# Kernel optimization log

Hardware: AMD Instinct MI355X
Metric: run time of the kernel (lower is better)

## Reference

```python
import jax, jax.numpy as jnp
import numpy as np

B, T, C, H = 8, 2048, 768, 64  # batch, seq, n_embed, head_size

def setup_inputs() -> dict:
    key = jax.random.key(0)
    kx, kq, kk, kv = jax.random.split(key, 4)
    x = jax.random.normal(kx, (B, T, C), dtype=jnp.float32)
    Wq = jax.random.normal(kq, (C, H), dtype=jnp.float32) * (C ** -0.5)
    Wk = jax.random.normal(kk, (C, H), dtype=jnp.float32) * (C ** -0.5)
    Wv = jax.random.normal(kv, (C, H), dtype=jnp.float32) * (C ** -0.5)
    return {"x": x, "Wq": Wq, "Wk": Wk, "Wv": Wv}

def reference(x, Wq, Wk, Wv):
    # projections (bias-free linears)
    q = jnp.einsum('btc,ch->bth', x, Wq)
    k = jnp.einsum('btc,ch->bth', x, Wk)
    v = jnp.einsum('btc,ch->bth', x, Wv)
    scale = k.shape[-1] ** -0.5
    wei = jnp.einsum('bth,bsh->bts', q, k) * scale  # [B, T, T]
    Tq = x.shape[1]
    causal = jnp.tril(jnp.ones((Tq, Tq), dtype=bool))
    wei = jnp.where(causal, wei, -jnp.inf)
    wei = jax.nn.softmax(wei, axis=-1)
    # dropout p=0.0 -> identity
    out = jnp.einsum('bts,bsh->bth', wei, v)
    return out
```

## Files before the change

kernel.cpp:

```cpp
#include <hip/hip_runtime.h>


typedef __bf16 bf16x8 __attribute__((ext_vector_type(8)));
typedef float  f32x4  __attribute__((ext_vector_type(4)));
typedef unsigned int u32;

union ABu {
    bf16x8 v;
    uint4  u;
    unsigned short us[8];
};

__device__ __forceinline__ unsigned short f2bf(float f) {
    union { __bf16 h; unsigned short s; } c;
    c.h = (__bf16)f;
    return c.s;
}
__device__ __forceinline__ float bf2f(unsigned short s) {
    union { unsigned int u; float f; } c; c.u = ((unsigned int)s) << 16;
    return c.f;
}
__device__ __forceinline__ u32 cvtpk_bf16(float lo, float hi) {
    u32 r;
    asm("v_cvt_pk_bf16_f32 %0, %1, %2" : "=v"(r) : "v"(lo), "v"(hi));
    return r;
}

__device__ __forceinline__ void gld16(void* lds, const void* g) {
    __builtin_amdgcn_global_load_lds(
        (const u32 __attribute__((address_space(1)))*)g,
        (u32 __attribute__((address_space(3)))*)lds, 16, 0, 0);
}

__global__ __launch_bounds__(256)
void wt_kernel(const float* __restrict__ Wq, const float* __restrict__ Wk,
               const float* __restrict__ Wv, unsigned short* __restrict__ wF) {
    const int j   = blockIdx.x / 6;
    const int kgg = blockIdx.x % 6;
    const int t = threadIdx.x;
    const int kg = kgg * 4 + (t >> 6);
    const int lane = t & 63, quad = lane >> 4, l16 = lane & 15;
    const int m = j >> 2, nb = (j & 3) * 16;
    const float* W = (m == 0) ? Wq : (m == 1) ? Wk : Wv;
    ABu o;
#pragma unroll
    for (int i = 0; i < 8; ++i)
        o.us[i] = f2bf(W[(kg * 32 + quad * 8 + i) * 64 + nb + l16]);
    *(uint4*)(wF + ((size_t)(j * 24 + kg) * 64 + lane) * 8) = o.u;
}

__global__ __launch_bounds__(512, 4)
void qkv_kernel(const float* __restrict__ x, const unsigned short* __restrict__ wF,
                unsigned short* __restrict__ qF, unsigned short* __restrict__ kF,
                unsigned short* __restrict__ vF) {
    __shared__ float          xs[2][32][68];
    __shared__ unsigned short wsW[2][24][64][8];
    __shared__ unsigned short Cst[2][12][16][17];
    const int tid  = threadIdx.x;
    const int lane = tid & 63, w = tid >> 6;
    const int l16  = lane & 15, quad = lane >> 4;
    const int mh   = w & 1, nh = w >> 1;
    const int m0   = blockIdx.x * 32;
    const int b    = m0 >> 11;

    f32x4 acc[3];
#pragma unroll
    for (int j = 0; j < 3; ++j) acc[j] = (f32x4){0.f, 0.f, 0.f, 0.f};

    const int xrow = tid >> 4, xc16 = tid & 15;

#pragma unroll
    for (int i = 0; i < 3; ++i) {
        const int c = w * 3 + i, j = c >> 1, kg2 = c & 1;
        gld16((char*)wsW[0] + (size_t)c * 1024 + lane * 16,
              (const char*)wF + ((size_t)(j * 24 + kg2) * 64 + lane) * 16);
    }
    *(float4*)&xs[0][xrow][xc16 * 4] =
        *(const float4*)&x[(size_t)(m0 + xrow) * 768 + xc16 * 4];
    __syncthreads();

    for (int kk = 0; kk < 12; ++kk) {
        const int cur = kk & 1, nxt = cur ^ 1;
        float4 xn;
        if (kk + 1 < 12) {
#pragma unroll
            for (int i = 0; i < 3; ++i) {
                const int c = w * 3 + i, j = c >> 1, kg2 = c & 1;
                gld16((char*)wsW[nxt] + (size_t)c * 1024 + lane * 16,
                      (const char*)wF + ((size_t)(j * 24 + (kk + 1) * 2 + kg2) * 64 + lane) * 16);
            }
            xn = *(const float4*)&x[(size_t)(m0 + xrow) * 768 + (kk + 1) * 64 + xc16 * 4];
        }

#pragma unroll
        for (int kg2 = 0; kg2 < 2; ++kg2) {
            const float* xr = &xs[cur][mh * 16 + l16][kg2 * 32 + quad * 8];
            float4 f0 = *(const float4*)xr;
            float4 f1 = *(const float4*)(xr + 4);
            ABu af;
            af.u.x = cvtpk_bf16(f0.x, f0.y);
            af.u.y = cvtpk_bf16(f0.z, f0.w);
            af.u.z = cvtpk_bf16(f1.x, f1.y);
            af.u.w = cvtpk_bf16(f1.z, f1.w);
#pragma unroll
            for (int jl = 0; jl < 3; ++jl) {
                const int j = nh * 3 + jl;
                ABu bf;
                bf.u = *(const uint4*)((char*)wsW[cur] + (size_t)(j * 2 + kg2) * 1024 + lane * 16);
                acc[jl] = __builtin_amdgcn_mfma_f32_16x16x32_bf16(af.v, bf.v, acc[jl], 0, 0, 0);
            }
        }

        if (kk + 1 < 12)
            *(float4*)&xs[nxt][xrow][xc16 * 4] = xn;
        __syncthreads();
    }

#pragma unroll
    for (int jl = 0; jl < 3; ++jl)
#pragma unroll
        for (int r = 0; r < 4; ++r)
            Cst[mh][nh * 3 + jl][quad * 4 + r][l16] = f2bf(acc[jl][r]);
    __syncthreads();

    const int g = tid >> 6, el = tid & 63;
    const int eq = el >> 4, e16 = el & 15;
    if (g < 4) {
        const int mhh = g >> 1, kg = g & 1;
        ABu oq, ok;
#pragma unroll
        for (int i = 0; i < 8; ++i) {
            const int h = kg * 32 + eq * 8 + i;
            oq.us[i] = Cst[mhh][h >> 4][e16][h & 15];
            ok.us[i] = Cst[mhh][4 + (h >> 4)][e16][h & 15];
        }
        const size_t tt = (size_t)b * 128 + ((m0 & 2047) >> 4) + mhh;
        *(uint4*)(qF + ((tt * 2 + kg) * 64 + el) * 8) = oq.u;
        *(uint4*)(kF + ((tt * 2 + kg) * 64 + el) * 8) = ok.u;
    } else {
        const int nt = g & 3;
        const int sv = (m0 & 2047) >> 6, kg = (m0 >> 5) & 1;
        ABu ov;
#pragma unroll
        for (int i = 0; i < 8; ++i) {
            const int loc = eq * 8 + i;
            ov.us[i] = Cst[loc >> 4][8 + nt][loc & 15][e16];
        }
        *(uint4*)(vF + ((((size_t)(b * 32 + sv) * 4 + nt) * 2 + kg) * 64 + el) * 8) = ov.u;
    }
}

template<bool MASKED>
__device__ __forceinline__ void attn_tile(
    const int st, const int b, const int tq0,
    const int lane, const int l16, const int quad,
    const ABu& aq0, const ABu& aq1,
    const unsigned short* __restrict__ kF,
    const unsigned short* __restrict__ vF,
    f32x4 acc[4], float& lsum)
{
    const float SC = 0.125f * 1.44269504089f;
    const float MB = 16.0f  * 1.44269504089f;
    const int s0 = st * 64;
    const unsigned short* kbase = kF + (size_t)(b * 128 + st * 4) * 1024;
    const unsigned short* vbase = vF + (size_t)(b * 32 + st) * 4096;

    ABu kf[8];
#pragma unroll
    for (int c = 0; c < 8; ++c)
        kf[c].u = *(const uint4*)(kbase + (size_t)c * 512 + lane * 8);

    float p[4][4];
#pragma unroll
    for (int nt = 0; nt < 4; ++nt) {
        f32x4 s = (f32x4){0.f, 0.f, 0.f, 0.f};
        s = __builtin_amdgcn_mfma_f32_16x16x32_bf16(kf[nt * 2 + 0].v, aq0.v, s, 0, 0, 0);
        s = __builtin_amdgcn_mfma_f32_16x16x32_bf16(kf[nt * 2 + 1].v, aq1.v, s, 0, 0, 0);
#pragma unroll
        for (int r = 0; r < 4; ++r) {
            float pv = __builtin_amdgcn_exp2f(__builtin_fmaf(s[r], SC, -MB));
            if (MASKED)
                pv = (s0 + nt * 16 + quad * 4 + r > tq0 + l16) ? 0.f : pv;
            p[nt][r] = pv;
            lsum += pv;
        }
    }

    ABu vf[8];
#pragma unroll
    for (int c = 0; c < 8; ++c)
        vf[c].u = *(const uint4*)(vbase + (size_t)c * 512 + lane * 8);

    ABu af[2];
#pragma unroll
    for (int ks = 0; ks < 2; ++ks) {
        u32 x0 = cvtpk_bf16(p[2 * ks][0], p[2 * ks][1]);
        u32 x1 = cvtpk_bf16(p[2 * ks][2], p[2 * ks][3]);
        u32 y0 = cvtpk_bf16(p[2 * ks + 1][0], p[2 * ks + 1][1]);
        u32 y1 = cvtpk_bf16(p[2 * ks + 1][2], p[2 * ks + 1][3]);
        asm("v_permlane32_swap_b32 %0, %1" : "+v"(x0), "+v"(y0));
        asm("v_permlane16_swap_b32 %0, %1" : "+v"(x0), "+v"(y0));
        asm("v_permlane32_swap_b32 %0, %1" : "+v"(x1), "+v"(y1));
        asm("v_permlane16_swap_b32 %0, %1" : "+v"(x1), "+v"(y1));
        af[ks].u = (uint4){x0, x1, y0, y1};
    }

#pragma unroll
    for (int nt = 0; nt < 4; ++nt) {
        acc[nt] = __builtin_amdgcn_mfma_f32_16x16x32_bf16(af[0].v, vf[nt * 2 + 0].v, acc[nt], 0, 0, 0);
        acc[nt] = __builtin_amdgcn_mfma_f32_16x16x32_bf16(af[1].v, vf[nt * 2 + 1].v, acc[nt], 0, 0, 0);
    }
}

__global__ __launch_bounds__(256, 4)
void attn_kernel(const unsigned short* __restrict__ qF,
                 const unsigned short* __restrict__ kF,
                 const unsigned short* __restrict__ vF,
                 unsigned short* __restrict__ opart, float* __restrict__ lpart) {
    const int tid  = threadIdx.x;
    const int lane = tid & 63, w = tid >> 6;
    const int l16  = lane & 15, quad = lane >> 4;
    const int idx  = blockIdx.x;
    const int b    = idx >> 7;
    const int rem  = idx & 127;
    const int jj   = rem >> 2, quarter = rem & 3;
    const int qs   = (jj & 1) ? (31 - (jj >> 1)) : (jj >> 1);
    const int tt   = qs * 4 + w;
    const int tq0  = tt * 16;

    ABu aq0, aq1;
    aq0.u = *(const uint4*)(qF + ((((size_t)b * 128 + tt) * 2 + 0) * 64 + lane) * 8);
    aq1.u = *(const uint4*)(qF + ((((size_t)b * 128 + tt) * 2 + 1) * 64 + lane) * 8);

    f32x4 acc[4];
#pragma unroll
    for (int nt = 0; nt < 4; ++nt) acc[nt] = (f32x4){0.f, 0.f, 0.f, 0.f};
    float lsum = 0.f;

    int st = quarter;
    for (; st < qs; st += 4)
        attn_tile<false>(st, b, tq0, lane, l16, quad, aq0, aq1, kF, vF, acc, lsum);
    if (st == qs)
        attn_tile<true>(st, b, tq0, lane, l16, quad, aq0, aq1, kF, vF, acc, lsum);

    lsum += __shfl_xor(lsum, 16);
    lsum += __shfl_xor(lsum, 32);

    unsigned short* obase = opart + ((size_t)(quarter * 8 + b) * 2048 + tq0) * 64;
#pragma unroll
    for (int nt = 0; nt < 4; ++nt)
#pragma unroll
        for (int r = 0; r < 4; ++r)
            obase[(size_t)(quad * 4 + r) * 64 + nt * 16 + l16] = f2bf(acc[nt][r]);
    if (lane < 16)
        lpart[(size_t)(quarter * 8 + b) * 2048 + tq0 + lane] = lsum;
}

__global__ __launch_bounds__(256)
void finalize_kernel(const unsigned short* __restrict__ opart,
                     const float* __restrict__ lpart, float* __restrict__ out) {
    const int idx = blockIdx.x * 256 + threadIdx.x;
    const int row = idx >> 4;
    float4 v = (float4){0.f, 0.f, 0.f, 0.f};
    float  l = 0.f;
#pragma unroll
    for (int q = 0; q < 4; ++q) {
        ushort4 u = ((const ushort4*)opart)[(size_t)q * 262144 + idx];
        v.x += bf2f(u.x); v.y += bf2f(u.y); v.z += bf2f(u.z); v.w += bf2f(u.w);
        l += lpart[(size_t)q * 16384 + row];
    }
    const float li = 1.f / l;
    v.x *= li; v.y *= li; v.z *= li; v.w *= li;
    ((float4*)out)[idx] = v;
}

extern "C" void kernel_launch(void* const* d_in, const int* in_sizes, int n_in,
                              void* d_out, int out_size, void* d_ws, size_t ws_size,
                              hipStream_t stream) {
    const float* x  = (const float*)d_in[0];
    const float* Wq = (const float*)d_in[1];
    const float* Wk = (const float*)d_in[2];
    const float* Wv = (const float*)d_in[3];
    float* out = (float*)d_out;

    char* ws = (char*)d_ws;
    unsigned short* wF    = (unsigned short*)ws;
    unsigned short* qF    = (unsigned short*)(ws + (512 << 10));
    unsigned short* kF    = (unsigned short*)(ws + (512 << 10) + (2 << 20));
    unsigned short* vF    = (unsigned short*)(ws + (512 << 10) + (4 << 20));
    unsigned short* opart = (unsigned short*)(ws + (512 << 10) + (6 << 20));
    float*          lpart = (float*)(ws + (512 << 10) + (14 << 20));

    wt_kernel<<<72, 256, 0, stream>>>(Wq, Wk, Wv, wF);
    qkv_kernel<<<512, 512, 0, stream>>>(x, wF, qF, kF, vF);
    attn_kernel<<<1024, 256, 0, stream>>>(qF, kF, vF, opart, lpart);
    finalize_kernel<<<1024, 256, 0, stream>>>(opart, lpart, out);
}
```

Measured before the change: 122.2 us.

## Store x as bf16 in LDS, compute row sums via MFMA, remap attention blocks

The QKV projection now converts x to bf16 once when writing it to shared memory, rather than converting per MFMA fragment read. This halves LDS footprint and read traffic for x. In attention, the softmax denominator is computed with an extra MFMA against a ones vector instead of scalar adds and cross-lane shuffles, so the sum now uses the bf16-rounded probabilities. The block-index mapping is also reordered so the batch index varies fastest, which changes scheduling and load balance across CUs.

```diff
diff --git a/kernel.cpp b/kernel.cpp
--- a/kernel.cpp
+++ b/kernel.cpp
@@ -53,7 +53,7 @@
 void qkv_kernel(const float* __restrict__ x, const unsigned short* __restrict__ wF,
                 unsigned short* __restrict__ qF, unsigned short* __restrict__ kF,
                 unsigned short* __restrict__ vF) {
-    __shared__ float          xs[2][32][68];
+    __shared__ unsigned short xs[2][32][72];
     __shared__ unsigned short wsW[2][24][64][8];
     __shared__ unsigned short Cst[2][12][16][17];
     const int tid  = threadIdx.x;
@@ -75,8 +75,11 @@
         gld16((char*)wsW[0] + (size_t)c * 1024 + lane * 16,
               (const char*)wF + ((size_t)(j * 24 + kg2) * 64 + lane) * 16);
     }
-    *(float4*)&xs[0][xrow][xc16 * 4] =
-        *(const float4*)&x[(size_t)(m0 + xrow) * 768 + xc16 * 4];
+    {
+        float4 xv = *(const float4*)&x[(size_t)(m0 + xrow) * 768 + xc16 * 4];
+        *(uint2*)&xs[0][xrow][xc16 * 4] =
+            (uint2){cvtpk_bf16(xv.x, xv.y), cvtpk_bf16(xv.z, xv.w)};
+    }
     __syncthreads();
 
     for (int kk = 0; kk < 12; ++kk) {
@@ -94,14 +97,8 @@
 
 #pragma unroll
         for (int kg2 = 0; kg2 < 2; ++kg2) {
-            const float* xr = &xs[cur][mh * 16 + l16][kg2 * 32 + quad * 8];
-            float4 f0 = *(const float4*)xr;
-            float4 f1 = *(const float4*)(xr + 4);
             ABu af;
-            af.u.x = cvtpk_bf16(f0.x, f0.y);
-            af.u.y = cvtpk_bf16(f0.z, f0.w);
-            af.u.z = cvtpk_bf16(f1.x, f1.y);
-            af.u.w = cvtpk_bf16(f1.z, f1.w);
+            af.u = *(const uint4*)&xs[cur][mh * 16 + l16][kg2 * 32 + quad * 8];
 #pragma unroll
             for (int jl = 0; jl < 3; ++jl) {
                 const int j = nh * 3 + jl;
@@ -112,7 +109,8 @@
         }
 
         if (kk + 1 < 12)
-            *(float4*)&xs[nxt][xrow][xc16 * 4] = xn;
+            *(uint2*)&xs[nxt][xrow][xc16 * 4] =
+                (uint2){cvtpk_bf16(xn.x, xn.y), cvtpk_bf16(xn.z, xn.w)};
         __syncthreads();
     }
 
@@ -154,10 +152,10 @@
 __device__ __forceinline__ void attn_tile(
     const int st, const int b, const int tq0,
     const int lane, const int l16, const int quad,
-    const ABu& aq0, const ABu& aq1,
+    const ABu& aq0, const ABu& aq1, const ABu& onesb,
     const unsigned short* __restrict__ kF,
     const unsigned short* __restrict__ vF,
-    f32x4 acc[4], float& lsum)
+    f32x4 acc[4], f32x4& lacc)
 {
     const float SC = 0.125f * 1.44269504089f;
     const float MB = 16.0f  * 1.44269504089f;
@@ -182,7 +180,6 @@
             if (MASKED)
                 pv = (s0 + nt * 16 + quad * 4 + r > tq0 + l16) ? 0.f : pv;
             p[nt][r] = pv;
-            lsum += pv;
         }
     }
 
@@ -210,6 +207,8 @@
         acc[nt] = __builtin_amdgcn_mfma_f32_16x16x32_bf16(af[0].v, vf[nt * 2 + 0].v, acc[nt], 0, 0, 0);
         acc[nt] = __builtin_amdgcn_mfma_f32_16x16x32_bf16(af[1].v, vf[nt * 2 + 1].v, acc[nt], 0, 0, 0);
     }
+    lacc = __builtin_amdgcn_mfma_f32_16x16x32_bf16(af[0].v, onesb.v, lacc, 0, 0, 0);
+    lacc = __builtin_amdgcn_mfma_f32_16x16x32_bf16(af[1].v, onesb.v, lacc, 0, 0, 0);
 }
 
 __global__ __launch_bounds__(256, 4)
@@ -221,30 +220,31 @@
     const int lane = tid & 63, w = tid >> 6;
     const int l16  = lane & 15, quad = lane >> 4;
     const int idx  = blockIdx.x;
-    const int b    = idx >> 7;
-    const int rem  = idx & 127;
-    const int jj   = rem >> 2, quarter = rem & 3;
-    const int qs   = (jj & 1) ? (31 - (jj >> 1)) : (jj >> 1);
+    const int b    = idx & 7;
+    const int hi   = idx >> 3;
+    const int quarter = hi & 3;
+    const int g    = (hi >> 2) & 7;
+    const int tr   = hi >> 5;
+    const int v    = g + ((tr >> 1) << 3);
+    const int qs   = (tr & 1) ? (31 - v) : v;
     const int tt   = qs * 4 + w;
     const int tq0  = tt * 16;
 
-    ABu aq0, aq1;
+    ABu aq0, aq1, onesb;
     aq0.u = *(const uint4*)(qF + ((((size_t)b * 128 + tt) * 2 + 0) * 64 + lane) * 8);
     aq1.u = *(const uint4*)(qF + ((((size_t)b * 128 + tt) * 2 + 1) * 64 + lane) * 8);
+    onesb.u = (uint4){0x3F803F80u, 0x3F803F80u, 0x3F803F80u, 0x3F803F80u};
 
     f32x4 acc[4];
 #pragma unroll
     for (int nt = 0; nt < 4; ++nt) acc[nt] = (f32x4){0.f, 0.f, 0.f, 0.f};
-    float lsum = 0.f;
+    f32x4 lacc = (f32x4){0.f, 0.f, 0.f, 0.f};
 
     int st = quarter;
     for (; st < qs; st += 4)
-        attn_tile<false>(st, b, tq0, lane, l16, quad, aq0, aq1, kF, vF, acc, lsum);
+        attn_tile<false>(st, b, tq0, lane, l16, quad, aq0, aq1, onesb, kF, vF, acc, lacc);
     if (st == qs)
-        attn_tile<true>(st, b, tq0, lane, l16, quad, aq0, aq1, kF, vF, acc, lsum);
-
-    lsum += __shfl_xor(lsum, 16);
-    lsum += __shfl_xor(lsum, 32);
+        attn_tile<true>(st, b, tq0, lane, l16, quad, aq0, aq1, onesb, kF, vF, acc, lacc);
 
     unsigned short* obase = opart + ((size_t)(quarter * 8 + b) * 2048 + tq0) * 64;
 #pragma unroll
@@ -252,8 +252,11 @@
 #pragma unroll
         for (int r = 0; r < 4; ++r)
             obase[(size_t)(quad * 4 + r) * 64 + nt * 16 + l16] = f2bf(acc[nt][r]);
-    if (lane < 16)
-        lpart[(size_t)(quarter * 8 + b) * 2048 + tq0 + lane] = lsum;
+    if (l16 == 0) {
+#pragma unroll
+        for (int r = 0; r < 4; ++r)
+            lpart[(size_t)(quarter * 8 + b) * 2048 + tq0 + quad * 4 + r] = lacc[r];
+    }
 }
 
 __global__ __launch_bounds__(256)
```

Measured after the change: 117.3 us. -4.0%, faster.
